# Performance work log

Measured on AMD Instinct MI355X. Metric: run time of the kernel, lower is better.

Reference implementation:

```python
import jax, jax.numpy as jnp
import numpy as np

N = 50000      # nodes
E = 800000     # edges (avg degree 16)
DIN = 128
H = 128
DOUT = 64


def setup_inputs() -> dict:
    key = jax.random.key(0)
    ks = jax.random.split(key, 8)
    x = jax.random.normal(ks[0], (N, DIN), dtype=jnp.float32)
    edge_index = jax.random.randint(ks[1], (2, E), 0, N, dtype=jnp.int32)
    def glorot(k, fi, fo):
        return jax.random.normal(k, (fi, fo), dtype=jnp.float32) * (1.0 / np.sqrt(fi))
    return {
        "x": x,
        "edge_index": edge_index,
        "W1": glorot(ks[2], DIN, H), "b1": jnp.zeros((H,), jnp.float32),
        "W2": glorot(ks[3], H, H),   "b2": jnp.zeros((H,), jnp.float32),
        "W3": glorot(ks[4], H, DOUT),"b3": jnp.zeros((DOUT,), jnp.float32),
    }


def reference(x, edge_index, W1, b1, W2, b2, W3, b3):
    n = x.shape[0]
    # GCNConv: add self-loops, symmetric degree normalization D^-1/2 (A+I) D^-1/2
    loop = jnp.arange(n, dtype=edge_index.dtype)
    src = jnp.concatenate([edge_index[0], loop])  # [E+N]
    dst = jnp.concatenate([edge_index[1], loop])
    deg = jax.ops.segment_sum(jnp.ones(src.shape, x.dtype), dst, num_segments=n)
    dinv = jnp.where(deg > 0, jax.lax.rsqrt(deg), 0.0)
    norm = dinv[src] * dinv[dst]  # [E+N]

    def conv(h, W, b):
        h = h @ W                                   # [N, out]
        msg = h[src] * norm[:, None]                # gather + scale
        return jax.ops.segment_sum(msg, dst, num_segments=n) + b

    # gelu after every layer except the last (forward breaks before act)
    h = jax.nn.gelu(conv(x, W1, b1), approximate=False)
    h = jax.nn.gelu(conv(h, W2, b2), approximate=False)
    return conv(h, W3, b3)
```

## Files before the change

kernel.cpp:

```cpp
#include <hip/hip_runtime.h>
#include <math.h>

#define NDIN 128
#define NHID 128
#define NDOUT 64

typedef _Float16 half2_t __attribute__((ext_vector_type(2)));
typedef _Float16 half4_t __attribute__((ext_vector_type(4)));
typedef _Float16 half8_t __attribute__((ext_vector_type(8)));
typedef float    float4v __attribute__((ext_vector_type(4)));

__device__ __forceinline__ float gelu_exact(float x) {
    return 0.5f * x * (1.0f + erff(x * 0.70710678118654752f));
}


__device__ void wtrans_tile(const float* __restrict__ W, _Float16* __restrict__ Wt,
                            int K, int N, int bx, int by) {
    __shared__ float tile[32][33];
    int tx = threadIdx.x & 31, ty = threadIdx.x >> 5;
    for (int i = 0; i < 32; i += 8) {
        int k = by * 32 + ty + i, nn = bx * 32 + tx;
        tile[ty + i][tx] = (k < K && nn < N) ? W[(size_t)k * N + nn] : 0.f;
    }
    __syncthreads();
    for (int i = 0; i < 32; i += 8) {
        int nn = bx * 32 + ty + i, k = by * 32 + tx;
        if (nn < N && k < K) Wt[(size_t)nn * K + k] = (_Float16)tile[tx][ty + i];
    }
}

__global__ __launch_bounds__(256) void prep0_kernel(
    const float* __restrict__ W1, _Float16* __restrict__ W1t,
    const float* __restrict__ W2, _Float16* __restrict__ W2t,
    const float* __restrict__ W3, _Float16* __restrict__ W3t,
    int* __restrict__ count, int* __restrict__ done, int n) {
    int b = blockIdx.x;
    if (b < 16) {
        wtrans_tile(W1, W1t, NDIN, NHID, b & 3, b >> 2);
    } else if (b < 32) {
        wtrans_tile(W2, W2t, NHID, NHID, (b - 16) & 3, (b - 16) >> 2);
    } else if (b < 40) {
        wtrans_tile(W3, W3t, NHID, NDOUT, (b - 32) & 1, (b - 32) >> 1);
    } else {
        int z = b - 40;
        int i = z * 256 + threadIdx.x;
        if (i < n) count[i] = 0;
        if (z == 0 && threadIdx.x == 0) *done = 0;
    }
}


__global__ void count_kernel(const int* __restrict__ dst, int* __restrict__ count, int E) {
    int e = blockIdx.x * blockDim.x + threadIdx.x;
    if (e < E) atomicAdd(&count[dst[e]], 1);
}


__global__ __launch_bounds__(256) void reduce_scanp_kernel(
    const int* __restrict__ count, int* __restrict__ blocksum, int* __restrict__ blockoff,
    int* __restrict__ rowptr, int* __restrict__ done, int nb, int n) {
    __shared__ int s[256];
    __shared__ int islast;
    int t = threadIdx.x;
    int i = blockIdx.x * 256 + t;
    s[t] = (i < n) ? count[i] : 0;
    __syncthreads();
    for (int off = 128; off > 0; off >>= 1) {
        if (t < off) s[t] += s[t + off];
        __syncthreads();
    }
    if (t == 0) {
        atomicExch(&blocksum[blockIdx.x], s[0]);
        __threadfence();
        int old = atomicAdd(done, 1);
        islast = (old == nb - 1) ? 1 : 0;
    }
    __syncthreads();
    if (!islast) return;
    __threadfence();
    int v = (t < nb) ? atomicAdd(&blocksum[t], 0) : 0;
    s[t] = v;
    __syncthreads();
    for (int off = 1; off < 256; off <<= 1) {
        int u = (t >= off) ? s[t - off] : 0;
        __syncthreads();
        s[t] += u;
        __syncthreads();
    }
    if (t < nb) blockoff[t] = s[t] - v;
    if (t == 255) rowptr[n] = s[255];
}


__global__ __launch_bounds__(256) void scan_blocks_kernel(
    const int* __restrict__ count, const int* __restrict__ blockoff,
    int* __restrict__ rowptr, float* __restrict__ dinv, int n) {
    __shared__ int s[256];
    int i = blockIdx.x * 256 + threadIdx.x;
    int v = (i < n) ? count[i] : 0;
    s[threadIdx.x] = v;
    __syncthreads();
    for (int off = 1; off < 256; off <<= 1) {
        int u = (threadIdx.x >= off) ? s[threadIdx.x - off] : 0;
        __syncthreads();
        s[threadIdx.x] += u;
        __syncthreads();
    }
    if (i < n) {
        rowptr[i] = blockoff[blockIdx.x] + s[threadIdx.x] - v;
        dinv[i] = rsqrtf((float)(v + 1));
    }
}


__global__ void fill_kernel(const int* __restrict__ src, const int* __restrict__ dst,
                            const float* __restrict__ dinv, const int* __restrict__ rowptr,
                            int* __restrict__ count, int2* __restrict__ adj, int E) {
    int e = blockIdx.x * blockDim.x + threadIdx.x;
    if (e >= E) return;
    int s = src[e], d = dst[e];
    int slot = atomicSub(&count[d], 1) - 1;
    int p = rowptr[d] + slot;
    adj[p] = make_int2(s, __float_as_int(dinv[s] * dinv[d]));
}


template <int BN, bool AF16>
__global__ __launch_bounds__(256) void gemm_mfma(
    const void* __restrict__ Aptr, const _Float16* __restrict__ Bt,
    _Float16* __restrict__ T, int M) {
    __shared__ _Float16 lds_a[64][136];
    __shared__ _Float16 lds_bt[BN][136];
    const int K = 128;
    int tid = threadIdx.x;
    int bm = blockIdx.x * 64;
    int wave = tid >> 6, lane = tid & 63;
    int m = lane & 15, quad = lane >> 4;

    if (AF16) {
        const _Float16* A = (const _Float16*)Aptr;
#pragma unroll
        for (int j = 0; j < 4; j++) {
            int c = tid + j * 256;
            int r = c >> 4, col = (c & 15) << 3;
            int grow = bm + r;
            uint4 v = make_uint4(0, 0, 0, 0);
            if (grow < M) v = *(const uint4*)(A + (size_t)grow * K + col);
            *(uint4*)&lds_a[r][col] = v;
        }
    } else {
        const float* A = (const float*)Aptr;
#pragma unroll
        for (int j = 0; j < 8; j++) {
            int c = tid + j * 256;
            int r = c >> 5, col = (c & 31) << 2;
            int grow = bm + r;
            float4 v = make_float4(0.f, 0.f, 0.f, 0.f);
            if (grow < M) v = *(const float4*)(A + (size_t)grow * K + col);
            half4_t h;
            h[0] = (_Float16)v.x; h[1] = (_Float16)v.y;
            h[2] = (_Float16)v.z; h[3] = (_Float16)v.w;
            *(half4_t*)&lds_a[r][col] = h;
        }
    }
    {
        const int chunks = BN * K / 8;
        for (int c = tid; c < chunks; c += 256) {
            int r = c >> 4, col = (c & 15) << 3;
            *(uint4*)&lds_bt[r][col] = *(const uint4*)(Bt + (size_t)r * K + col);
        }
    }
    __syncthreads();

    const int NT = BN / 16;
    float4v acc[NT];
#pragma unroll
    for (int nt = 0; nt < NT; nt++) acc[nt] = (float4v){0.f, 0.f, 0.f, 0.f};

    int arow = (wave << 4) + m;
#pragma unroll
    for (int kc = 0; kc < K; kc += 32) {
        half8_t a = *(const half8_t*)&lds_a[arow][kc + quad * 8];
#pragma unroll
        for (int nt = 0; nt < NT; nt++) {
            half8_t b = *(const half8_t*)&lds_bt[nt * 16 + m][kc + quad * 8];
            acc[nt] = __builtin_amdgcn_mfma_f32_16x16x32_f16(a, b, acc[nt], 0, 0, 0);
        }
    }
#pragma unroll
    for (int nt = 0; nt < NT; nt++) {
#pragma unroll
        for (int r = 0; r < 4; r++) {
            int grow = bm + (wave << 4) + (quad << 2) + r;
            if (grow < M) T[(size_t)grow * BN + nt * 16 + m] = (_Float16)acc[nt][r];
        }
    }
}


template <int F, bool DOGELU, bool OUTF16>
__global__ __launch_bounds__(256) void agg_kernel(
    const _Float16* __restrict__ t, const int* __restrict__ rowptr,
    const int2* __restrict__ adj, const float* __restrict__ dinv,
    const float* __restrict__ bias, void* __restrict__ outp, int n) {
    int node = (int)((blockIdx.x * blockDim.x + threadIdx.x) >> 6);
    int lane = threadIdx.x & 63;
    if (node >= n) return;

    float wself = dinv[node];
    wself *= wself;
    int beg = rowptr[node];
    int end = rowptr[node + 1];

    if (F == 128) {
        const half2_t* t2 = (const half2_t*)t;
        half2_t v = t2[(size_t)node * 64 + lane];
        float accx = wself * (float)v[0], accy = wself * (float)v[1];
        for (int e0 = beg; e0 < end; e0 += 64) {
            int rem = end - e0;
            int j = 0; float w = 0.f;
            if (lane < rem) {
                int2 ed = adj[e0 + lane];
                j = ed.x; w = __int_as_float(ed.y);
            }
            int cnt = rem < 64 ? rem : 64;
            for (int c = 0; c < cnt; c += 16) {
#pragma unroll
                for (int i = 0; i < 16; i++) {
                    int jj = __builtin_amdgcn_readlane(j, c + i);
                    float ww = __int_as_float(
                        __builtin_amdgcn_readlane(__float_as_int(w), c + i));
                    half2_t u = t2[(size_t)jj * 64 + lane];
                    accx += ww * (float)u[0];
                    accy += ww * (float)u[1];
                }
            }
        }
        float2 b = ((const float2*)bias)[lane];
        accx += b.x; accy += b.y;
        if (DOGELU) { accx = gelu_exact(accx); accy = gelu_exact(accy); }
        if (OUTF16) {
            half2_t o; o[0] = (_Float16)accx; o[1] = (_Float16)accy;
            ((half2_t*)outp)[(size_t)node * 64 + lane] = o;
        } else {
            float2 o; o.x = accx; o.y = accy;
            ((float2*)outp)[(size_t)node * 64 + lane] = o;
        }
    } else {
        float acc = wself * (float)t[(size_t)node * 64 + lane];
        for (int e0 = beg; e0 < end; e0 += 64) {
            int rem = end - e0;
            int j = 0; float w = 0.f;
            if (lane < rem) {
                int2 ed = adj[e0 + lane];
                j = ed.x; w = __int_as_float(ed.y);
            }
            int cnt = rem < 64 ? rem : 64;
            for (int c = 0; c < cnt; c += 16) {
#pragma unroll
                for (int i = 0; i < 16; i++) {
                    int jj = __builtin_amdgcn_readlane(j, c + i);
                    float ww = __int_as_float(
                        __builtin_amdgcn_readlane(__float_as_int(w), c + i));
                    acc += ww * (float)t[(size_t)jj * 64 + lane];
                }
            }
        }
        acc += bias[lane];
        if (DOGELU) acc = gelu_exact(acc);
        if (OUTF16) ((_Float16*)outp)[(size_t)node * 64 + lane] = (_Float16)acc;
        else        ((float*)outp)[(size_t)node * 64 + lane] = acc;
    }
}


extern "C" void kernel_launch(void* const* d_in, const int* in_sizes, int n_in,
                              void* d_out, int out_size, void* d_ws, size_t ws_size,
                              hipStream_t stream) {
    const float* x  = (const float*)d_in[0];
    const int* edge = (const int*)d_in[1];
    const float* W1 = (const float*)d_in[2];
    const float* b1 = (const float*)d_in[3];
    const float* W2 = (const float*)d_in[4];
    const float* b2 = (const float*)d_in[5];
    const float* W3 = (const float*)d_in[6];
    const float* b3 = (const float*)d_in[7];
    float* out = (float*)d_out;

    const int N = in_sizes[0] / NDIN;
    const int E = in_sizes[1] / 2;
    const int* src = edge;
    const int* dst = edge + E;
    const int NB = (N + 255) / 256;

    char* p = (char*)d_ws;
    auto alloc = [&](size_t bytes) {
        char* q = p;
        p += (bytes + 255) & ~(size_t)255;
        return q;
    };
    int*       count    = (int*)alloc((size_t)N * 4);
    int*       rowptr   = (int*)alloc((size_t)(N + 1) * 4);
    int*       blocksum = (int*)alloc((size_t)NB * 4);
    int*       blockoff = (int*)alloc((size_t)NB * 4);
    int*       done     = (int*)alloc(256);
    float*     dinv     = (float*)alloc((size_t)N * 4);
    int2*      adj      = (int2*)alloc((size_t)E * 8);
    _Float16*  W1t      = (_Float16*)alloc((size_t)NHID * NDIN * 2);
    _Float16*  W2t      = (_Float16*)alloc((size_t)NHID * NHID * 2);
    _Float16*  W3t      = (_Float16*)alloc((size_t)NDOUT * NHID * 2);
    _Float16*  tbuf     = (_Float16*)alloc((size_t)N * NHID * 2);
    _Float16*  hbuf     = (_Float16*)alloc((size_t)N * NHID * 2);

    dim3 blk(256);
    int mtiles = (N + 63) / 64;
    int eblocks = (E + 255) / 256;
    int agg_blocks = (N + 3) / 4;

    prep0_kernel<<<40 + NB, blk, 0, stream>>>(W1, W1t, W2, W2t, W3, W3t, count, done, N);
    count_kernel<<<eblocks, blk, 0, stream>>>(dst, count, E);
    reduce_scanp_kernel<<<NB, blk, 0, stream>>>(count, blocksum, blockoff, rowptr,
                                                done, NB, N);
    scan_blocks_kernel<<<NB, blk, 0, stream>>>(count, blockoff, rowptr, dinv, N);
    fill_kernel<<<eblocks, blk, 0, stream>>>(src, dst, dinv, rowptr, count, adj, E);
    gemm_mfma<128, false><<<mtiles, blk, 0, stream>>>(x, W1t, tbuf, N);
    agg_kernel<128, true, true><<<agg_blocks, blk, 0, stream>>>(tbuf, rowptr, adj,
                                                                dinv, b1, hbuf, N);
    gemm_mfma<128, true><<<mtiles, blk, 0, stream>>>(hbuf, W2t, tbuf, N);
    agg_kernel<128, true, true><<<agg_blocks, blk, 0, stream>>>(tbuf, rowptr, adj,
                                                                dinv, b2, hbuf, N);
    gemm_mfma<64, true><<<mtiles, blk, 0, stream>>>(hbuf, W3t, tbuf, N);
    agg_kernel<64, false, false><<<agg_blocks, blk, 0, stream>>>(tbuf, rowptr, adj,
                                                                 dinv, b3, out, N);
}
```

Measured before the change: 293.8 us.

## Fuse graph scans, fill with first GEMM, and aggregation with following GEMMs

The two scan kernels become one. Blocks other than the last spin on a global flag until the last block has written the block offsets, which assumes every block is resident at once. Edge fill and the first GEMM share one launch through a block-index split. The layer-1 and layer-2 aggregations now write their GELU outputs into LDS and feed the next layer's MFMA GEMM directly, with weights read from global memory instead of LDS. This cuts kernel launches and the intermediate hidden-buffer round trip, but each wave now aggregates 16 nodes in sequence, so far fewer waves run the gather-bound aggregation in parallel.

```diff
diff --git a/kernel.cpp b/kernel.cpp
--- a/kernel.cpp
+++ b/kernel.cpp
@@ -46,7 +46,7 @@
         int z = b - 40;
         int i = z * 256 + threadIdx.x;
         if (i < n) count[i] = 0;
-        if (z == 0 && threadIdx.x == 0) *done = 0;
+        if (z == 0 && threadIdx.x < 64) done[threadIdx.x] = 0;
     }
 }
 
@@ -57,14 +57,17 @@
 }
 
 
-__global__ __launch_bounds__(256) void reduce_scanp_kernel(
+__global__ __launch_bounds__(256) void reduce_scan_kernel(
     const int* __restrict__ count, int* __restrict__ blocksum, int* __restrict__ blockoff,
-    int* __restrict__ rowptr, int* __restrict__ done, int nb, int n) {
+    int* __restrict__ rowptr, float* __restrict__ dinv, int* __restrict__ done,
+    int nb, int n) {
     __shared__ int s[256];
-    __shared__ int islast;
+    __shared__ int flag;
+    __shared__ int boff_s;
     int t = threadIdx.x;
     int i = blockIdx.x * 256 + t;
-    s[t] = (i < n) ? count[i] : 0;
+    int v = (i < n) ? count[i] : 0;
+    s[t] = v;
     __syncthreads();
     for (int off = 128; off > 0; off >>= 1) {
         if (t < off) s[t] += s[t + off];
@@ -73,13 +76,31 @@
     if (t == 0) {
         atomicExch(&blocksum[blockIdx.x], s[0]);
         __threadfence();
-        int old = atomicAdd(done, 1);
-        islast = (old == nb - 1) ? 1 : 0;
-    }
-    __syncthreads();
-    if (!islast) return;
-    __threadfence();
-    int v = (t < nb) ? atomicAdd(&blocksum[t], 0) : 0;
+        int old = atomicAdd(&done[0], 1);
+        flag = (old == nb - 1) ? 1 : 0;
+    }
+    __syncthreads();
+    if (flag) {
+        __threadfence();
+        int pv = (t < nb) ? atomicAdd(&blocksum[t], 0) : 0;
+        s[t] = pv;
+        __syncthreads();
+        for (int off = 1; off < 256; off <<= 1) {
+            int u = (t >= off) ? s[t - off] : 0;
+            __syncthreads();
+            s[t] += u;
+            __syncthreads();
+        }
+        if (t < nb) atomicExch(&blockoff[t], s[t] - pv);
+        if (t == 255) rowptr[n] = s[255];
+        __threadfence();
+        if (t == 0) atomicExch(&done[1], 1);
+    } else if (t == 0) {
+        while (atomicAdd(&done[1], 0) == 0) __builtin_amdgcn_s_sleep(2);
+        __threadfence();
+    }
+    __syncthreads();
+    if (t == 0) boff_s = atomicAdd(&blockoff[blockIdx.x], 0);
     s[t] = v;
     __syncthreads();
     for (int off = 1; off < 256; off <<= 1) {
@@ -88,103 +109,31 @@
         s[t] += u;
         __syncthreads();
     }
-    if (t < nb) blockoff[t] = s[t] - v;
-    if (t == 255) rowptr[n] = s[255];
-}
-
-
-__global__ __launch_bounds__(256) void scan_blocks_kernel(
-    const int* __restrict__ count, const int* __restrict__ blockoff,
-    int* __restrict__ rowptr, float* __restrict__ dinv, int n) {
-    __shared__ int s[256];
-    int i = blockIdx.x * 256 + threadIdx.x;
-    int v = (i < n) ? count[i] : 0;
-    s[threadIdx.x] = v;
-    __syncthreads();
-    for (int off = 1; off < 256; off <<= 1) {
-        int u = (threadIdx.x >= off) ? s[threadIdx.x - off] : 0;
-        __syncthreads();
-        s[threadIdx.x] += u;
-        __syncthreads();
-    }
     if (i < n) {
-        rowptr[i] = blockoff[blockIdx.x] + s[threadIdx.x] - v;
+        rowptr[i] = boff_s + s[t] - v;
         dinv[i] = rsqrtf((float)(v + 1));
     }
 }
 
 
-__global__ void fill_kernel(const int* __restrict__ src, const int* __restrict__ dst,
-                            const float* __restrict__ dinv, const int* __restrict__ rowptr,
-                            int* __restrict__ count, int2* __restrict__ adj, int E) {
-    int e = blockIdx.x * blockDim.x + threadIdx.x;
-    if (e >= E) return;
-    int s = src[e], d = dst[e];
-    int slot = atomicSub(&count[d], 1) - 1;
-    int p = rowptr[d] + slot;
-    adj[p] = make_int2(s, __float_as_int(dinv[s] * dinv[d]));
-}
-
-
-template <int BN, bool AF16>
-__global__ __launch_bounds__(256) void gemm_mfma(
-    const void* __restrict__ Aptr, const _Float16* __restrict__ Bt,
-    _Float16* __restrict__ T, int M) {
-    __shared__ _Float16 lds_a[64][136];
-    __shared__ _Float16 lds_bt[BN][136];
-    const int K = 128;
+template <int BN>
+__device__ __forceinline__ void gemm_phaseB(
+    const _Float16 (*lds_a)[136], const _Float16* __restrict__ Bt,
+    _Float16* __restrict__ T, int bm, int M) {
     int tid = threadIdx.x;
-    int bm = blockIdx.x * 64;
     int wave = tid >> 6, lane = tid & 63;
     int m = lane & 15, quad = lane >> 4;
-
-    if (AF16) {
-        const _Float16* A = (const _Float16*)Aptr;
-#pragma unroll
-        for (int j = 0; j < 4; j++) {
-            int c = tid + j * 256;
-            int r = c >> 4, col = (c & 15) << 3;
-            int grow = bm + r;
-            uint4 v = make_uint4(0, 0, 0, 0);
-            if (grow < M) v = *(const uint4*)(A + (size_t)grow * K + col);
-            *(uint4*)&lds_a[r][col] = v;
-        }
-    } else {
-        const float* A = (const float*)Aptr;
-#pragma unroll
-        for (int j = 0; j < 8; j++) {
-            int c = tid + j * 256;
-            int r = c >> 5, col = (c & 31) << 2;
-            int grow = bm + r;
-            float4 v = make_float4(0.f, 0.f, 0.f, 0.f);
-            if (grow < M) v = *(const float4*)(A + (size_t)grow * K + col);
-            half4_t h;
-            h[0] = (_Float16)v.x; h[1] = (_Float16)v.y;
-            h[2] = (_Float16)v.z; h[3] = (_Float16)v.w;
-            *(half4_t*)&lds_a[r][col] = h;
-        }
-    }
-    {
-        const int chunks = BN * K / 8;
-        for (int c = tid; c < chunks; c += 256) {
-            int r = c >> 4, col = (c & 15) << 3;
-            *(uint4*)&lds_bt[r][col] = *(const uint4*)(Bt + (size_t)r * K + col);
-        }
-    }
-    __syncthreads();
-
     const int NT = BN / 16;
     float4v acc[NT];
 #pragma unroll
     for (int nt = 0; nt < NT; nt++) acc[nt] = (float4v){0.f, 0.f, 0.f, 0.f};
-
     int arow = (wave << 4) + m;
 #pragma unroll
-    for (int kc = 0; kc < K; kc += 32) {
+    for (int kc = 0; kc < 128; kc += 32) {
         half8_t a = *(const half8_t*)&lds_a[arow][kc + quad * 8];
 #pragma unroll
         for (int nt = 0; nt < NT; nt++) {
-            half8_t b = *(const half8_t*)&lds_bt[nt * 16 + m][kc + quad * 8];
+            half8_t b = *(const half8_t*)&Bt[(size_t)(nt * 16 + m) * 128 + kc + quad * 8];
             acc[nt] = __builtin_amdgcn_mfma_f32_16x16x32_f16(a, b, acc[nt], 0, 0, 0);
         }
     }
@@ -196,6 +145,104 @@
             if (grow < M) T[(size_t)grow * BN + nt * 16 + m] = (_Float16)acc[nt][r];
         }
     }
+}
+
+
+__device__ __forceinline__ half2_t agg_node128(
+    const half2_t* __restrict__ t2, const int* __restrict__ rowptr,
+    const int2* __restrict__ adj, const float* __restrict__ dinv,
+    const float* __restrict__ bias, int node, int lane) {
+    float wself = dinv[node];
+    wself *= wself;
+    half2_t v = t2[(size_t)node * 64 + lane];
+    float accx = wself * (float)v[0], accy = wself * (float)v[1];
+    int beg = rowptr[node], end = rowptr[node + 1];
+    for (int e0 = beg; e0 < end; e0 += 64) {
+        int rem = end - e0;
+        int j = 0; float w = 0.f;
+        if (lane < rem) {
+            int2 ed = adj[e0 + lane];
+            j = ed.x; w = __int_as_float(ed.y);
+        }
+        int cnt = rem < 64 ? rem : 64;
+        for (int c = 0; c < cnt; c += 16) {
+#pragma unroll
+            for (int i = 0; i < 16; i++) {
+                int jj = __builtin_amdgcn_readlane(j, c + i);
+                float ww = __int_as_float(
+                    __builtin_amdgcn_readlane(__float_as_int(w), c + i));
+                half2_t u = t2[(size_t)jj * 64 + lane];
+                accx += ww * (float)u[0];
+                accy += ww * (float)u[1];
+            }
+        }
+    }
+    float2 b = ((const float2*)bias)[lane];
+    accx = gelu_exact(accx + b.x);
+    accy = gelu_exact(accy + b.y);
+    half2_t o; o[0] = (_Float16)accx; o[1] = (_Float16)accy;
+    return o;
+}
+
+
+__global__ __launch_bounds__(256) void fill_gemm1_kernel(
+    const int* __restrict__ src, const int* __restrict__ dst,
+    const float* __restrict__ dinv, const int* __restrict__ rowptr,
+    int* __restrict__ count, int2* __restrict__ adj, int E,
+    const float* __restrict__ x, const _Float16* __restrict__ W1t,
+    _Float16* __restrict__ T, int M, int fillblocks) {
+    __shared__ _Float16 lds_a[64][136];
+    int b = blockIdx.x;
+    if (b < fillblocks) {
+        int e = b * 256 + threadIdx.x;
+        if (e >= E) return;
+        int s = src[e], d = dst[e];
+        int slot = atomicSub(&count[d], 1) - 1;
+        int p = rowptr[d] + slot;
+        adj[p] = make_int2(s, __float_as_int(dinv[s] * dinv[d]));
+        return;
+    }
+    int bm = (b - fillblocks) * 64;
+    int tid = threadIdx.x;
+#pragma unroll
+    for (int j = 0; j < 8; j++) {
+        int c = tid + j * 256;
+        int r = c >> 5, col = (c & 31) << 2;
+        int grow = bm + r;
+        float4 v = make_float4(0.f, 0.f, 0.f, 0.f);
+        if (grow < M) v = *(const float4*)(x + (size_t)grow * 128 + col);
+        half4_t h;
+        h[0] = (_Float16)v.x; h[1] = (_Float16)v.y;
+        h[2] = (_Float16)v.z; h[3] = (_Float16)v.w;
+        *(half4_t*)&lds_a[r][col] = h;
+    }
+    __syncthreads();
+    gemm_phaseB<128>(lds_a, W1t, T, bm, M);
+}
+
+
+template <int BN>
+__global__ __launch_bounds__(256, 4) void agg_gemm_kernel(
+    const _Float16* __restrict__ t, const int* __restrict__ rowptr,
+    const int2* __restrict__ adj, const float* __restrict__ dinv,
+    const float* __restrict__ bias, const _Float16* __restrict__ Bt,
+    _Float16* __restrict__ T, int M) {
+    __shared__ _Float16 lds_a[64][136];
+    int tid = threadIdx.x;
+    int wave = tid >> 6, lane = tid & 63;
+    int bm = blockIdx.x * 64;
+    const half2_t* t2 = (const half2_t*)t;
+#pragma unroll 1
+    for (int p = 0; p < 16; p++) {
+        int r = (wave << 4) + p;
+        int node = bm + r;
+        half2_t o;
+        o[0] = (_Float16)0.f; o[1] = (_Float16)0.f;
+        if (node < M) o = agg_node128(t2, rowptr, adj, dinv, bias, node, lane);
+        *(half2_t*)&lds_a[r][lane << 1] = o;
+    }
+    __syncthreads();
+    gemm_phaseB<BN>(lds_a, Bt, T, bm, M);
 }
 
 
@@ -320,17 +367,14 @@
 
     prep0_kernel<<<40 + NB, blk, 0, stream>>>(W1, W1t, W2, W2t, W3, W3t, count, done, N);
     count_kernel<<<eblocks, blk, 0, stream>>>(dst, count, E);
-    reduce_scanp_kernel<<<NB, blk, 0, stream>>>(count, blocksum, blockoff, rowptr,
-                                                done, NB, N);
-    scan_blocks_kernel<<<NB, blk, 0, stream>>>(count, blockoff, rowptr, dinv, N);
-    fill_kernel<<<eblocks, blk, 0, stream>>>(src, dst, dinv, rowptr, count, adj, E);
-    gemm_mfma<128, false><<<mtiles, blk, 0, stream>>>(x, W1t, tbuf, N);
-    agg_kernel<128, true, true><<<agg_blocks, blk, 0, stream>>>(tbuf, rowptr, adj,
-                                                                dinv, b1, hbuf, N);
-    gemm_mfma<128, true><<<mtiles, blk, 0, stream>>>(hbuf, W2t, tbuf, N);
-    agg_kernel<128, true, true><<<agg_blocks, blk, 0, stream>>>(tbuf, rowptr, adj,
-                                                                dinv, b2, hbuf, N);
-    gemm_mfma<64, true><<<mtiles, blk, 0, stream>>>(hbuf, W3t, tbuf, N);
+    reduce_scan_kernel<<<NB, blk, 0, stream>>>(count, blocksum, blockoff, rowptr,
+                                               dinv, done, NB, N);
+    fill_gemm1_kernel<<<eblocks + mtiles, blk, 0, stream>>>(
+        src, dst, dinv, rowptr, count, adj, E, x, W1t, tbuf, N, eblocks);
+    agg_gemm_kernel<128><<<mtiles, blk, 0, stream>>>(tbuf, rowptr, adj, dinv, b1,
+                                                     W2t, hbuf, N);
+    agg_gemm_kernel<64><<<mtiles, blk, 0, stream>>>(hbuf, rowptr, adj, dinv, b2,
+                                                    W3t, tbuf, N);
     agg_kernel<64, false, false><<<agg_blocks, blk, 0, stream>>>(tbuf, rowptr, adj,
                                                                  dinv, b3, out, N);
 }
```

Measured after the change: 324.3 us. 10.4% more time.
